# Kernel tuning notes

Measured on AMD Instinct MI355X. Metric: run time of the kernel, lower is better.

Reference implementation:

```python
import jax, jax.numpy as jnp
import numpy as np

N = 1048576  # rays * samples per batch
IN_DIM = 32          # hashgrid encoder output (16 levels x 2 feats)
SH_DIM = 16          # degree-4 spherical harmonics
HID = 64
GEO = 15


def sh_encode(v):
    """Real spherical harmonics up to degree 4 (16 comps), v: [N,3] unit vecs."""
    x, y, z = v[..., 0], v[..., 1], v[..., 2]
    xx, yy, zz = x * x, y * y, z * z
    xy, yz, xz = x * y, y * z, x * z
    comps = [
        jnp.full_like(x, 0.28209479177387814),
        -0.48860251190291987 * y,
        0.48860251190291987 * z,
        -0.48860251190291987 * x,
        1.0925484305920792 * xy,
        -1.0925484305920792 * yz,
        0.94617469575755997 * zz - 0.31539156525252005,
        -1.0925484305920792 * xz,
        0.54627421529603959 * (xx - yy),
        0.59004358992664352 * y * (3.0 * xx - yy),
        2.8906114426405538 * xy * z,
        0.45704579946446572 * y * (4.0 * zz - xx - yy),
        0.3731763325901154 * z * (2.0 * zz - 3.0 * xx - 3.0 * yy),
        0.45704579946446572 * x * (4.0 * zz - xx - yy),
        1.445305721320277 * z * (xx - yy),
        0.5900435899266435 * x * (xx - 3.0 * yy),
    ]
    return jnp.stack(comps, axis=-1)


def _w(key, fan_in, fan_out):
    return jax.random.normal(key, (fan_in, fan_out), dtype=jnp.float32) / np.sqrt(fan_in)


def setup_inputs() -> dict:
    key = jax.random.key(0)
    ks = jax.random.split(key, 12)
    x_feat = jax.random.normal(ks[0], (N, IN_DIM), dtype=jnp.float32)
    d = jax.random.normal(ks[1], (N, 3), dtype=jnp.float32)
    d = d / jnp.linalg.norm(d, axis=-1, keepdims=True)
    lig = jax.random.normal(ks[2], (N, 3), dtype=jnp.float32)
    lig = lig / jnp.linalg.norm(lig, axis=-1, keepdims=True)
    return {
        "x_feat": x_feat, "d": d, "lig": lig,
        # sigma net: 32 -> 64 -> 1+15
        "w_sig0": _w(ks[3], IN_DIM, HID),
        "w_sig1": _w(ks[4], HID, 1 + GEO),
        # color net: (16+16+32) -> 64, (64+15) -> 64, 64 -> 3
        "w_col0": _w(ks[5], SH_DIM + SH_DIM + IN_DIM, HID),
        "w_col1": _w(ks[6], HID + GEO, HID),
        "w_col2": _w(ks[7], HID, 3),
        # vis net (only 2 layers run in forward): (16+32) -> 64, 64 -> 1
        "w_vis0": _w(ks[8], SH_DIM + IN_DIM, HID),
        "w_vis1": _w(ks[9], HID, 1),
    }


def reference(x_feat, d, lig, w_sig0, w_sig1, w_col0, w_col1, w_col2, w_vis0, w_vis1):
    # sigma tower (bias-free)
    h = jax.nn.relu(x_feat @ w_sig0)
    h = h @ w_sig1                      # [N, 1+GEO]
    geo_feat = h[..., 1:]               # sigma = trunc_exp(h[...,0]) is unused in output

    d_enc = sh_encode(d)                # [N,16]
    l_enc = sh_encode(lig)              # [N,16]

    # color tower: cat([h_x, light, d]) then cat geo_feat before layer 1
    hc = jnp.concatenate([x_feat, l_enc, d_enc], axis=-1)
    hc = jax.nn.relu(hc @ w_col0)
    hc = jnp.concatenate([hc, geo_feat], axis=-1)
    hc = jax.nn.relu(hc @ w_col1)
    hc = hc @ w_col2
    color = jax.nn.relu(hc)             # [N,3]

    # vis tower: cat([h_x, light]), 2 layers (range(num_layers))
    hv = jnp.concatenate([x_feat, l_enc], axis=-1)
    hv = jax.nn.relu(hv @ w_vis0)
    hv = hv @ w_vis1
    vis = jax.nn.sigmoid(hv)            # [N,1]

    return color * vis                  # broadcast -> [N,3]
```

## Files before the change

### kernel.cpp

```cpp
#include <hip/hip_runtime.h>
#include <math.h>

#define BLOCK 256
#define GRID  2048

typedef _Float16 half8 __attribute__((ext_vector_type(8)));
typedef float    f32x4 __attribute__((ext_vector_type(4)));

__device__ __forceinline__ int phi(int nt, int m) {
    return ((nt >> 1) << 5) + ((m >> 2) << 3) + ((nt & 1) << 2) + (m & 3);
}

__device__ __forceinline__ half8 bfragW(const float* __restrict__ w, int N0,
                                        int nsrc, int k0, int Kreal, bool valid) {
    half8 r;
    #pragma unroll
    for (int j = 0; j < 8; j++) {
        int k = k0 + j;
        float v = (valid && k < Kreal) ? w[k * N0 + nsrc] : 0.f;
        r[j] = (_Float16)v;
    }
    return r;
}

__device__ __forceinline__ half8 packrelu(f32x4 a, f32x4 b) {
    half8 h;
    #pragma unroll
    for (int r = 0; r < 4; r++) {
        h[r]     = (_Float16)fmaxf(a[r], 0.f);
        h[4 + r] = (_Float16)fmaxf(b[r], 0.f);
    }
    return h;
}

__device__ __forceinline__ half8 packraw(f32x4 a, f32x4 b) {
    half8 h;
    #pragma unroll
    for (int r = 0; r < 4; r++) {
        h[r]     = (_Float16)a[r];
        h[4 + r] = (_Float16)b[r];
    }
    return h;
}

__device__ __forceinline__ void sh16(float x, float y, float z, float* e) {
    float xx = x * x, yy = y * y, zz = z * z;
    float xy = x * y, yz = y * z, xz = x * z;
    e[0]  = 0.28209479177387814f;
    e[1]  = -0.48860251190291987f * y;
    e[2]  = 0.48860251190291987f * z;
    e[3]  = -0.48860251190291987f * x;
    e[4]  = 1.0925484305920792f * xy;
    e[5]  = -1.0925484305920792f * yz;
    e[6]  = 0.94617469575756f * zz - 0.31539156525252005f;
    e[7]  = -1.0925484305920792f * xz;
    e[8]  = 0.5462742152960396f * (xx - yy);
    e[9]  = 0.5900435899266435f * y * (3.0f * xx - yy);
    e[10] = 2.890611442640554f * xy * z;
    e[11] = 0.4570457994644657f * y * (4.0f * zz - xx - yy);
    e[12] = 0.3731763325901154f * z * (2.0f * zz - 3.0f * xx - 3.0f * yy);
    e[13] = 0.4570457994644657f * x * (4.0f * zz - xx - yy);
    e[14] = 1.445305721320277f * z * (xx - yy);
    e[15] = 0.5900435899266435f * x * (xx - 3.0f * yy);
}

#define MFMA(A, B, C) __builtin_amdgcn_mfma_f32_16x16x32_f16((A), (B), (C), 0, 0, 0)
#define SBAR() __builtin_amdgcn_sched_barrier(0)

#define NFRAG  40
#define F_SIG0 0
#define F_COL0 4
#define F_VIS0 12
#define F_SIG1 20
#define F_VIS1 24
#define F_COL1 26
#define F_COL2 38

__global__ __launch_bounds__(BLOCK, 2) void nerf_dual2(
    const float* __restrict__ x_feat,
    const float* __restrict__ dvec,
    const float* __restrict__ lvec,
    const float* __restrict__ w_sig0,
    const float* __restrict__ w_sig1,
    const float* __restrict__ w_col0,
    const float* __restrict__ w_col1,
    const float* __restrict__ w_col2,
    const float* __restrict__ w_vis0,
    const float* __restrict__ w_vis1,
    float* __restrict__ out, int n)
{
    const int tid  = threadIdx.x;
    const int wv   = tid >> 6;
    const int lane = tid & 63;
    const int m    = lane & 15;
    const int q    = lane >> 4;

    __shared__ half8 WL[NFRAG * 64];

    if (wv == 0) {
        #pragma unroll
        for (int nt = 0; nt < 4; nt++)
            WL[(F_SIG0 + nt) * 64 + lane] =
                bfragW(w_sig0, 64, phi(nt, m), q * 8, 32, true);
        #pragma unroll
        for (int nt = 0; nt < 2; nt++)
            #pragma unroll
            for (int kt = 0; kt < 2; kt++) {
                int g = ((m >> 2) << 3) + ((nt & 1) << 2) + (m & 3);
                bool valid = ((m >> 2) < 2) && (g < 15);
                WL[(F_SIG1 + nt * 2 + kt) * 64 + lane] =
                    bfragW(w_sig1, 16, g + 1, kt * 32 + q * 8, 64, valid);
            }
        #pragma unroll
        for (int kt = 0; kt < 2; kt++)
            WL[(F_VIS1 + kt) * 64 + lane] =
                bfragW(w_vis1, 1, 0, kt * 32 + q * 8, 64, m == 0);
    } else if (wv == 1) {
        #pragma unroll
        for (int nt = 0; nt < 4; nt++)
            #pragma unroll
            for (int kt = 0; kt < 2; kt++)
                WL[(F_COL0 + nt * 2 + kt) * 64 + lane] =
                    bfragW(w_col0, 64, phi(nt, m), kt * 32 + q * 8, 64, true);
        #pragma unroll
        for (int kt = 0; kt < 2; kt++)
            WL[(F_COL2 + kt) * 64 + lane] =
                bfragW(w_col2, 3, m, kt * 32 + q * 8, 64, m < 3);
    } else if (wv == 2) {
        #pragma unroll
        for (int nt = 0; nt < 4; nt++)
            #pragma unroll
            for (int kt = 0; kt < 2; kt++)
                WL[(F_VIS0 + nt * 2 + kt) * 64 + lane] =
                    bfragW(w_vis0, 64, phi(nt, m), kt * 32 + q * 8, 48, true);
    } else {
        #pragma unroll
        for (int nt = 0; nt < 4; nt++)
            #pragma unroll
            for (int kt = 0; kt < 3; kt++)
                WL[(F_COL1 + nt * 3 + kt) * 64 + lane] =
                    bfragW(w_col1, 64, phi(nt, m), kt * 32 + q * 8, 79, true);
    }
    __syncthreads();

    int wl = lane;
    #define LW(f) WL[wl + (f) * 64]

    const f32x4 z = {0.f, 0.f, 0.f, 0.f};
    const int ntiles = n >> 7;
    for (int t = blockIdx.x; t < ntiles; t += GRID) {
        asm volatile("" : "+v"(wl));

        const int pt0 = (t << 7) + wv * 32 + m;
        const int pt1 = pt0 + 16;

        half8 fA0, fA1;
        {
            const float4* xa = (const float4*)(x_feat + (size_t)pt0 * 32 + q * 8);
            float4 v0 = xa[0], v1 = xa[1];
            fA0[0] = (_Float16)v0.x; fA0[1] = (_Float16)v0.y;
            fA0[2] = (_Float16)v0.z; fA0[3] = (_Float16)v0.w;
            fA0[4] = (_Float16)v1.x; fA0[5] = (_Float16)v1.y;
            fA0[6] = (_Float16)v1.z; fA0[7] = (_Float16)v1.w;
            const float* va = (q < 2 ? lvec : dvec) + (size_t)pt0 * 3;
            float e[16];
            sh16(va[0], va[1], va[2], e);
            #pragma unroll
            for (int u = 0; u < 8; u++) {
                float s = (q & 1) ? e[8 + u] : e[u];
                fA1[u] = (_Float16)s;
            }
        }
        half8 fB0, fB1;
        {
            const float4* xb = (const float4*)(x_feat + (size_t)pt1 * 32 + q * 8);
            float4 u0 = xb[0], u1 = xb[1];
            fB0[0] = (_Float16)u0.x; fB0[1] = (_Float16)u0.y;
            fB0[2] = (_Float16)u0.z; fB0[3] = (_Float16)u0.w;
            fB0[4] = (_Float16)u1.x; fB0[5] = (_Float16)u1.y;
            fB0[6] = (_Float16)u1.z; fB0[7] = (_Float16)u1.w;
            const float* vb = (q < 2 ? lvec : dvec) + (size_t)pt1 * 3;
            float e[16];
            sh16(vb[0], vb[1], vb[2], e);
            #pragma unroll
            for (int u = 0; u < 8; u++) {
                float s = (q & 1) ? e[8 + u] : e[u];
                fB1[u] = (_Float16)s;
            }
        }
        SBAR();

        half8 w;
        f32x4 aA, aB, bA, bB;

        w = LW(F_SIG0 + 0); aA = MFMA(w, fA0, z); aB = MFMA(w, fB0, z);
        w = LW(F_SIG0 + 1); bA = MFMA(w, fA0, z); bB = MFMA(w, fB0, z);
        half8 hK0a = packrelu(aA, bA), hK0b = packrelu(aB, bB);
        w = LW(F_SIG0 + 2); aA = MFMA(w, fA0, z); aB = MFMA(w, fB0, z);
        w = LW(F_SIG0 + 3); bA = MFMA(w, fA0, z); bB = MFMA(w, fB0, z);
        half8 hK1a = packrelu(aA, bA), hK1b = packrelu(aB, bB);
        SBAR();

        aA = z; aB = z; bA = z; bB = z;
        w = LW(F_SIG1 + 0); aA = MFMA(w, hK0a, aA); aB = MFMA(w, hK0b, aB);
        w = LW(F_SIG1 + 1); aA = MFMA(w, hK1a, aA); aB = MFMA(w, hK1b, aB);
        w = LW(F_SIG1 + 2); bA = MFMA(w, hK0a, bA); bB = MFMA(w, hK0b, bB);
        w = LW(F_SIG1 + 3); bA = MFMA(w, hK1a, bA); bB = MFMA(w, hK1b, bB);
        half8 gA = packraw(aA, bA), gB = packraw(aB, bB);
        SBAR();

        aA = z; aB = z; bA = z; bB = z;
        w = LW(F_COL0 + 0); aA = MFMA(w, fA0, aA); aB = MFMA(w, fB0, aB);
        w = LW(F_COL0 + 1); aA = MFMA(w, fA1, aA); aB = MFMA(w, fB1, aB);
        w = LW(F_COL0 + 2); bA = MFMA(w, fA0, bA); bB = MFMA(w, fB0, bB);
        w = LW(F_COL0 + 3); bA = MFMA(w, fA1, bA); bB = MFMA(w, fB1, bB);
        half8 cK0a = packrelu(aA, bA), cK0b = packrelu(aB, bB);
        aA = z; aB = z; bA = z; bB = z;
        w = LW(F_COL0 + 4); aA = MFMA(w, fA0, aA); aB = MFMA(w, fB0, aB);
        w = LW(F_COL0 + 5); aA = MFMA(w, fA1, aA); aB = MFMA(w, fB1, aB);
        w = LW(F_COL0 + 6); bA = MFMA(w, fA0, bA); bB = MFMA(w, fB0, bB);
        w = LW(F_COL0 + 7); bA = MFMA(w, fA1, bA); bB = MFMA(w, fB1, bB);
        half8 cK1a = packrelu(aA, bA), cK1b = packrelu(aB, bB);
        SBAR();

        aA = z; aB = z; bA = z; bB = z;
        w = LW(F_VIS0 + 0); aA = MFMA(w, fA0, aA); aB = MFMA(w, fB0, aB);
        w = LW(F_VIS0 + 1); aA = MFMA(w, fA1, aA); aB = MFMA(w, fB1, aB);
        w = LW(F_VIS0 + 2); bA = MFMA(w, fA0, bA); bB = MFMA(w, fB0, bB);
        w = LW(F_VIS0 + 3); bA = MFMA(w, fA1, bA); bB = MFMA(w, fB1, bB);
        half8 vK0a = packrelu(aA, bA), vK0b = packrelu(aB, bB);
        aA = z; aB = z; bA = z; bB = z;
        w = LW(F_VIS0 + 4); aA = MFMA(w, fA0, aA); aB = MFMA(w, fB0, aB);
        w = LW(F_VIS0 + 5); aA = MFMA(w, fA1, aA); aB = MFMA(w, fB1, aB);
        w = LW(F_VIS0 + 6); bA = MFMA(w, fA0, bA); bB = MFMA(w, fB0, bB);
        w = LW(F_VIS0 + 7); bA = MFMA(w, fA1, bA); bB = MFMA(w, fB1, bB);
        half8 vK1a = packrelu(aA, bA), vK1b = packrelu(aB, bB);

        f32x4 va = z, vb = z;
        w = LW(F_VIS1 + 0); va = MFMA(w, vK0a, va); vb = MFMA(w, vK0b, vb);
        w = LW(F_VIS1 + 1); va = MFMA(w, vK1a, va); vb = MFMA(w, vK1b, vb);
        float visA = 1.f / (1.f + expf(-va[0]));
        float visB = 1.f / (1.f + expf(-vb[0]));
        SBAR();

        aA = z; aB = z; bA = z; bB = z;
        w = LW(F_COL1 + 0);  aA = MFMA(w, cK0a, aA); aB = MFMA(w, cK0b, aB);
        w = LW(F_COL1 + 1);  aA = MFMA(w, cK1a, aA); aB = MFMA(w, cK1b, aB);
        w = LW(F_COL1 + 2);  aA = MFMA(w, gA,   aA); aB = MFMA(w, gB,   aB);
        w = LW(F_COL1 + 3);  bA = MFMA(w, cK0a, bA); bB = MFMA(w, cK0b, bB);
        w = LW(F_COL1 + 4);  bA = MFMA(w, cK1a, bA); bB = MFMA(w, cK1b, bB);
        w = LW(F_COL1 + 5);  bA = MFMA(w, gA,   bA); bB = MFMA(w, gB,   bB);
        half8 h2K0a = packrelu(aA, bA), h2K0b = packrelu(aB, bB);
        aA = z; aB = z; bA = z; bB = z;
        w = LW(F_COL1 + 6);  aA = MFMA(w, cK0a, aA); aB = MFMA(w, cK0b, aB);
        w = LW(F_COL1 + 7);  aA = MFMA(w, cK1a, aA); aB = MFMA(w, cK1b, aB);
        w = LW(F_COL1 + 8);  aA = MFMA(w, gA,   aA); aB = MFMA(w, gB,   aB);
        w = LW(F_COL1 + 9);  bA = MFMA(w, cK0a, bA); bB = MFMA(w, cK0b, bB);
        w = LW(F_COL1 + 10); bA = MFMA(w, cK1a, bA); bB = MFMA(w, cK1b, bB);
        w = LW(F_COL1 + 11); bA = MFMA(w, gA,   bA); bB = MFMA(w, gB,   bB);
        half8 h2K1a = packrelu(aA, bA), h2K1b = packrelu(aB, bB);
        SBAR();

        f32x4 ca = z, cb = z;
        w = LW(F_COL2 + 0); ca = MFMA(w, h2K0a, ca); cb = MFMA(w, h2K0b, cb);
        w = LW(F_COL2 + 1); ca = MFMA(w, h2K1a, ca); cb = MFMA(w, h2K1b, cb);
        if (q == 0) {
            float* oa = out + (size_t)pt0 * 3;
            oa[0] = fmaxf(ca[0], 0.f) * visA;
            oa[1] = fmaxf(ca[1], 0.f) * visA;
            oa[2] = fmaxf(ca[2], 0.f) * visA;
            float* ob = out + (size_t)pt1 * 3;
            ob[0] = fmaxf(cb[0], 0.f) * visB;
            ob[1] = fmaxf(cb[1], 0.f) * visB;
            ob[2] = fmaxf(cb[2], 0.f) * visB;
        }
    }
    #undef LW
}

extern "C" void kernel_launch(void* const* d_in, const int* in_sizes, int n_in,
                              void* d_out, int out_size, void* d_ws, size_t ws_size,
                              hipStream_t stream) {
    const float* x_feat = (const float*)d_in[0];
    const float* dvec   = (const float*)d_in[1];
    const float* lvec   = (const float*)d_in[2];
    const float* w_sig0 = (const float*)d_in[3];
    const float* w_sig1 = (const float*)d_in[4];
    const float* w_col0 = (const float*)d_in[5];
    const float* w_col1 = (const float*)d_in[6];
    const float* w_col2 = (const float*)d_in[7];
    const float* w_vis0 = (const float*)d_in[8];
    const float* w_vis1 = (const float*)d_in[9];
    float* out = (float*)d_out;

    const int n = in_sizes[0] / 32;
    nerf_dual2<<<GRID, BLOCK, 0, stream>>>(x_feat, dvec, lvec,
                                           w_sig0, w_sig1, w_col0, w_col1,
                                           w_col2, w_vis0, w_vis1, out, n);
}
```

Before: 270.0 us.

## Software-prefetch next tile's inputs into registers and raise occupancy hint

Loads the next tile's x_feat and direction/light vectors into registers while the current tile's MFMA chain runs, and issues the first tile's loads before the shared-memory weight staging. The goal is to hide global-memory latency behind compute. It also raises launch_bounds minimum blocks from 2 to 3, which tightens the register budget and risks spills given the extra prefetch registers. It drops the sched barrier after input prep and seeds accumulators directly with zero.

```diff
diff --git a/kernel.cpp b/kernel.cpp
--- a/kernel.cpp
+++ b/kernel.cpp
@@ -43,25 +43,44 @@
     return h;
 }
 
-__device__ __forceinline__ void sh16(float x, float y, float z, float* e) {
+__device__ __forceinline__ half8 shfrag(float x, float y, float z, bool hi) {
     float xx = x * x, yy = y * y, zz = z * z;
     float xy = x * y, yz = y * z, xz = x * z;
-    e[0]  = 0.28209479177387814f;
-    e[1]  = -0.48860251190291987f * y;
-    e[2]  = 0.48860251190291987f * z;
-    e[3]  = -0.48860251190291987f * x;
-    e[4]  = 1.0925484305920792f * xy;
-    e[5]  = -1.0925484305920792f * yz;
-    e[6]  = 0.94617469575756f * zz - 0.31539156525252005f;
-    e[7]  = -1.0925484305920792f * xz;
-    e[8]  = 0.5462742152960396f * (xx - yy);
-    e[9]  = 0.5900435899266435f * y * (3.0f * xx - yy);
-    e[10] = 2.890611442640554f * xy * z;
-    e[11] = 0.4570457994644657f * y * (4.0f * zz - xx - yy);
-    e[12] = 0.3731763325901154f * z * (2.0f * zz - 3.0f * xx - 3.0f * yy);
-    e[13] = 0.4570457994644657f * x * (4.0f * zz - xx - yy);
-    e[14] = 1.445305721320277f * z * (xx - yy);
-    e[15] = 0.5900435899266435f * x * (xx - 3.0f * yy);
+    float e0  = 0.28209479177387814f;
+    float e1  = -0.48860251190291987f * y;
+    float e2  = 0.48860251190291987f * z;
+    float e3  = -0.48860251190291987f * x;
+    float e4  = 1.0925484305920792f * xy;
+    float e5  = -1.0925484305920792f * yz;
+    float e6  = 0.94617469575756f * zz - 0.31539156525252005f;
+    float e7  = -1.0925484305920792f * xz;
+    float e8  = 0.5462742152960396f * (xx - yy);
+    float e9  = 0.5900435899266435f * y * (3.0f * xx - yy);
+    float e10 = 2.890611442640554f * xy * z;
+    float e11 = 0.4570457994644657f * y * (4.0f * zz - xx - yy);
+    float e12 = 0.3731763325901154f * z * (2.0f * zz - 3.0f * xx - 3.0f * yy);
+    float e13 = 0.4570457994644657f * x * (4.0f * zz - xx - yy);
+    float e14 = 1.445305721320277f * z * (xx - yy);
+    float e15 = 0.5900435899266435f * x * (xx - 3.0f * yy);
+    half8 r;
+    r[0] = (_Float16)(hi ? e8  : e0);
+    r[1] = (_Float16)(hi ? e9  : e1);
+    r[2] = (_Float16)(hi ? e10 : e2);
+    r[3] = (_Float16)(hi ? e11 : e3);
+    r[4] = (_Float16)(hi ? e12 : e4);
+    r[5] = (_Float16)(hi ? e13 : e5);
+    r[6] = (_Float16)(hi ? e14 : e6);
+    r[7] = (_Float16)(hi ? e15 : e7);
+    return r;
+}
+
+__device__ __forceinline__ half8 cvt8(float4 v0, float4 v1) {
+    half8 f;
+    f[0] = (_Float16)v0.x; f[1] = (_Float16)v0.y;
+    f[2] = (_Float16)v0.z; f[3] = (_Float16)v0.w;
+    f[4] = (_Float16)v1.x; f[5] = (_Float16)v1.y;
+    f[6] = (_Float16)v1.z; f[7] = (_Float16)v1.w;
+    return f;
 }
 
 #define MFMA(A, B, C) __builtin_amdgcn_mfma_f32_16x16x32_f16((A), (B), (C), 0, 0, 0)
@@ -76,7 +95,7 @@
 #define F_COL1 26
 #define F_COL2 38
 
-__global__ __launch_bounds__(BLOCK, 2) void nerf_dual2(
+__global__ __launch_bounds__(BLOCK, 3) void nerf_pf(
     const float* __restrict__ x_feat,
     const float* __restrict__ dvec,
     const float* __restrict__ lvec,
@@ -97,6 +116,25 @@
 
     __shared__ half8 WL[NFRAG * 64];
 
+    const float* dl = (q < 2) ? lvec : dvec;
+    const int ntiles = n >> 7;
+
+    float4 rxa0, rxa1, rxb0, rxb1;
+    float rvax, rvay, rvaz, rvbx, rvby, rvbz;
+    {
+        const int t0  = blockIdx.x;
+        const int pt0 = (t0 << 7) + wv * 32 + m;
+        const int pt1 = pt0 + 16;
+        const float4* xa = (const float4*)(x_feat + (size_t)pt0 * 32 + q * 8);
+        rxa0 = xa[0]; rxa1 = xa[1];
+        const float4* xb = (const float4*)(x_feat + (size_t)pt1 * 32 + q * 8);
+        rxb0 = xb[0]; rxb1 = xb[1];
+        const float* va = dl + (size_t)pt0 * 3;
+        rvax = va[0]; rvay = va[1]; rvaz = va[2];
+        const float* vb = dl + (size_t)pt1 * 3;
+        rvbx = vb[0]; rvby = vb[1]; rvbz = vb[2];
+    }
+
     if (wv == 0) {
         #pragma unroll
         for (int nt = 0; nt < 4; nt++)
@@ -147,48 +185,31 @@
     #define LW(f) WL[wl + (f) * 64]
 
     const f32x4 z = {0.f, 0.f, 0.f, 0.f};
-    const int ntiles = n >> 7;
     for (int t = blockIdx.x; t < ntiles; t += GRID) {
         asm volatile("" : "+v"(wl));
 
         const int pt0 = (t << 7) + wv * 32 + m;
         const int pt1 = pt0 + 16;
 
-        half8 fA0, fA1;
+        half8 fA0 = cvt8(rxa0, rxa1);
+        half8 fB0 = cvt8(rxb0, rxb1);
+        half8 fA1 = shfrag(rvax, rvay, rvaz, (q & 1) != 0);
+        half8 fB1 = shfrag(rvbx, rvby, rvbz, (q & 1) != 0);
+
         {
-            const float4* xa = (const float4*)(x_feat + (size_t)pt0 * 32 + q * 8);
-            float4 v0 = xa[0], v1 = xa[1];
-            fA0[0] = (_Float16)v0.x; fA0[1] = (_Float16)v0.y;
-            fA0[2] = (_Float16)v0.z; fA0[3] = (_Float16)v0.w;
-            fA0[4] = (_Float16)v1.x; fA0[5] = (_Float16)v1.y;
-            fA0[6] = (_Float16)v1.z; fA0[7] = (_Float16)v1.w;
-            const float* va = (q < 2 ? lvec : dvec) + (size_t)pt0 * 3;
-            float e[16];
-            sh16(va[0], va[1], va[2], e);
-            #pragma unroll
-            for (int u = 0; u < 8; u++) {
-                float s = (q & 1) ? e[8 + u] : e[u];
-                fA1[u] = (_Float16)s;
-            }
+            int tn = t + GRID;
+            int tp = (tn < ntiles) ? tn : t;
+            const int qt0 = (tp << 7) + wv * 32 + m;
+            const int qt1 = qt0 + 16;
+            const float4* xa = (const float4*)(x_feat + (size_t)qt0 * 32 + q * 8);
+            rxa0 = xa[0]; rxa1 = xa[1];
+            const float4* xb = (const float4*)(x_feat + (size_t)qt1 * 32 + q * 8);
+            rxb0 = xb[0]; rxb1 = xb[1];
+            const float* va = dl + (size_t)qt0 * 3;
+            rvax = va[0]; rvay = va[1]; rvaz = va[2];
+            const float* vb = dl + (size_t)qt1 * 3;
+            rvbx = vb[0]; rvby = vb[1]; rvbz = vb[2];
         }
-        half8 fB0, fB1;
-        {
-            const float4* xb = (const float4*)(x_feat + (size_t)pt1 * 32 + q * 8);
-            float4 u0 = xb[0], u1 = xb[1];
-            fB0[0] = (_Float16)u0.x; fB0[1] = (_Float16)u0.y;
-            fB0[2] = (_Float16)u0.z; fB0[3] = (_Float16)u0.w;
-            fB0[4] = (_Float16)u1.x; fB0[5] = (_Float16)u1.y;
-            fB0[6] = (_Float16)u1.z; fB0[7] = (_Float16)u1.w;
-            const float* vb = (q < 2 ? lvec : dvec) + (size_t)pt1 * 3;
-            float e[16];
-            sh16(vb[0], vb[1], vb[2], e);
-            #pragma unroll
-            for (int u = 0; u < 8; u++) {
-                float s = (q & 1) ? e[8 + u] : e[u];
-                fB1[u] = (_Float16)s;
-            }
-        }
-        SBAR();
 
         half8 w;
         f32x4 aA, aB, bA, bB;
@@ -201,38 +222,33 @@
         half8 hK1a = packrelu(aA, bA), hK1b = packrelu(aB, bB);
         SBAR();
 
-        aA = z; aB = z; bA = z; bB = z;
-        w = LW(F_SIG1 + 0); aA = MFMA(w, hK0a, aA); aB = MFMA(w, hK0b, aB);
+        w = LW(F_SIG1 + 0); aA = MFMA(w, hK0a, z);  aB = MFMA(w, hK0b, z);
         w = LW(F_SIG1 + 1); aA = MFMA(w, hK1a, aA); aB = MFMA(w, hK1b, aB);
-        w = LW(F_SIG1 + 2); bA = MFMA(w, hK0a, bA); bB = MFMA(w, hK0b, bB);
+        w = LW(F_SIG1 + 2); bA = MFMA(w, hK0a, z);  bB = MFMA(w, hK0b, z);
         w = LW(F_SIG1 + 3); bA = MFMA(w, hK1a, bA); bB = MFMA(w, hK1b, bB);
         half8 gA = packraw(aA, bA), gB = packraw(aB, bB);
         SBAR();
 
-        aA = z; aB = z; bA = z; bB = z;
-        w = LW(F_COL0 + 0); aA = MFMA(w, fA0, aA); aB = MFMA(w, fB0, aB);
+        w = LW(F_COL0 + 0); aA = MFMA(w, fA0, z);  aB = MFMA(w, fB0, z);
         w = LW(F_COL0 + 1); aA = MFMA(w, fA1, aA); aB = MFMA(w, fB1, aB);
-        w = LW(F_COL0 + 2); bA = MFMA(w, fA0, bA); bB = MFMA(w, fB0, bB);
+        w = LW(F_COL0 + 2); bA = MFMA(w, fA0, z);  bB = MFMA(w, fB0, z);
         w = LW(F_COL0 + 3); bA = MFMA(w, fA1, bA); bB = MFMA(w, fB1, bB);
         half8 cK0a = packrelu(aA, bA), cK0b = packrelu(aB, bB);
-        aA = z; aB = z; bA = z; bB = z;
-        w = LW(F_COL0 + 4); aA = MFMA(w, fA0, aA); aB = MFMA(w, fB0, aB);
+        w = LW(F_COL0 + 4); aA = MFMA(w, fA0, z);  aB = MFMA(w, fB0, z);
         w = LW(F_COL0 + 5); aA = MFMA(w, fA1, aA); aB = MFMA(w, fB1, aB);
-        w = LW(F_COL0 + 6); bA = MFMA(w, fA0, bA); bB = MFMA(w, fB0, bB);
+        w = LW(F_COL0 + 6); bA = MFMA(w, fA0, z);  bB = MFMA(w, fB0, z);
         w = LW(F_COL0 + 7); bA = MFMA(w, fA1, bA); bB = MFMA(w, fB1, bB);
         half8 cK1a = packrelu(aA, bA), cK1b = packrelu(aB, bB);
         SBAR();
 
-        aA = z; aB = z; bA = z; bB = z;
-        w = LW(F_VIS0 + 0); aA = MFMA(w, fA0, aA); aB = MFMA(w, fB0, aB);
+        w = LW(F_VIS0 + 0); aA = MFMA(w, fA0, z);  aB = MFMA(w, fB0, z);
         w = LW(F_VIS0 + 1); aA = MFMA(w, fA1, aA); aB = MFMA(w, fB1, aB);
-        w = LW(F_VIS0 + 2); bA = MFMA(w, fA0, bA); bB = MFMA(w, fB0, bB);
+        w = LW(F_VIS0 + 2); bA = MFMA(w, fA0, z);  bB = MFMA(w, fB0, z);
         w = LW(F_VIS0 + 3); bA = MFMA(w, fA1, bA); bB = MFMA(w, fB1, bB);
         half8 vK0a = packrelu(aA, bA), vK0b = packrelu(aB, bB);
-        aA = z; aB = z; bA = z; bB = z;
-        w = LW(F_VIS0 + 4); aA = MFMA(w, fA0, aA); aB = MFMA(w, fB0, aB);
+        w = LW(F_VIS0 + 4); aA = MFMA(w, fA0, z);  aB = MFMA(w, fB0, z);
         w = LW(F_VIS0 + 5); aA = MFMA(w, fA1, aA); aB = MFMA(w, fB1, aB);
-        w = LW(F_VIS0 + 6); bA = MFMA(w, fA0, bA); bB = MFMA(w, fB0, bB);
+        w = LW(F_VIS0 + 6); bA = MFMA(w, fA0, z);  bB = MFMA(w, fB0, z);
         w = LW(F_VIS0 + 7); bA = MFMA(w, fA1, bA); bB = MFMA(w, fB1, bB);
         half8 vK1a = packrelu(aA, bA), vK1b = packrelu(aB, bB);
 
@@ -243,19 +259,17 @@
         float visB = 1.f / (1.f + expf(-vb[0]));
         SBAR();
 
-        aA = z; aB = z; bA = z; bB = z;
-        w = LW(F_COL1 + 0);  aA = MFMA(w, cK0a, aA); aB = MFMA(w, cK0b, aB);
+        w = LW(F_COL1 + 0);  aA = MFMA(w, cK0a, z);  aB = MFMA(w, cK0b, z);
         w = LW(F_COL1 + 1);  aA = MFMA(w, cK1a, aA); aB = MFMA(w, cK1b, aB);
         w = LW(F_COL1 + 2);  aA = MFMA(w, gA,   aA); aB = MFMA(w, gB,   aB);
-        w = LW(F_COL1 + 3);  bA = MFMA(w, cK0a, bA); bB = MFMA(w, cK0b, bB);
+        w = LW(F_COL1 + 3);  bA = MFMA(w, cK0a, z);  bB = MFMA(w, cK0b, z);
         w = LW(F_COL1 + 4);  bA = MFMA(w, cK1a, bA); bB = MFMA(w, cK1b, bB);
         w = LW(F_COL1 + 5);  bA = MFMA(w, gA,   bA); bB = MFMA(w, gB,   bB);
         half8 h2K0a = packrelu(aA, bA), h2K0b = packrelu(aB, bB);
-        aA = z; aB = z; bA = z; bB = z;
-        w = LW(F_COL1 + 6);  aA = MFMA(w, cK0a, aA); aB = MFMA(w, cK0b, aB);
+        w = LW(F_COL1 + 6);  aA = MFMA(w, cK0a, z);  aB = MFMA(w, cK0b, z);
         w = LW(F_COL1 + 7);  aA = MFMA(w, cK1a, aA); aB = MFMA(w, cK1b, aB);
         w = LW(F_COL1 + 8);  aA = MFMA(w, gA,   aA); aB = MFMA(w, gB,   aB);
-        w = LW(F_COL1 + 9);  bA = MFMA(w, cK0a, bA); bB = MFMA(w, cK0b, bB);
+        w = LW(F_COL1 + 9);  bA = MFMA(w, cK0a, z);  bB = MFMA(w, cK0b, z);
         w = LW(F_COL1 + 10); bA = MFMA(w, cK1a, bA); bB = MFMA(w, cK1b, bB);
         w = LW(F_COL1 + 11); bA = MFMA(w, gA,   bA); bB = MFMA(w, gB,   bB);
         half8 h2K1a = packrelu(aA, bA), h2K1b = packrelu(aB, bB);
@@ -294,7 +308,7 @@
     float* out = (float*)d_out;
 
     const int n = in_sizes[0] / 32;
-    nerf_dual2<<<GRID, BLOCK, 0, stream>>>(x_feat, dvec, lvec,
-                                           w_sig0, w_sig1, w_col0, w_col1,
-                                           w_col2, w_vis0, w_vis1, out, n);
-}
+    nerf_pf<<<GRID, BLOCK, 0, stream>>>(x_feat, dvec, lvec,
+                                        w_sig0, w_sig1, w_col0, w_col1,
+                                        w_col2, w_vis0, w_vis1, out, n);
+}
```

Measured after the change: 239.4 us. 1.13x faster.
